# Kernel tuning notes

Hardware: AMD Instinct MI355X
Metric: run time of the kernel (lower is better)

Reference implementation:

```python
import jax, jax.numpy as jnp
import numpy as np

N, D, C, G, NNZ = 256, 1024, 50000, 4, 300000
EPS = 1e-5


def setup_inputs() -> dict:
    key = jax.random.key(0)
    ks = jax.random.split(key, 5)
    return {
        "output": jax.random.normal(ks[0], (N, D), jnp.float32),
        "wt2_w": jax.random.normal(ks[1], (C, D), jnp.float32) * 0.02,
        "wt2_b": jnp.zeros((C,), jnp.float32),
        "A_vals": jax.random.uniform(ks[2], (G, NNZ), dtype=jnp.float32),
        "vec": jnp.ones((G,), jnp.float32),
        "A_rows": jax.random.randint(ks[3], (G, NNZ), 0, C, jnp.int32),
        "A_cols": jax.random.randint(ks[4], (G, NNZ), 0, C, jnp.int32),
    }


def reference(output, wt2_w, wt2_b, A_vals, vec, A_rows, A_cols):
    # BatchNorm1d(embed_dim, affine=False), training-mode batch stats (biased var)
    mean = jnp.mean(output, axis=0)
    var = jnp.var(output, axis=0)
    h0 = (output - mean) * jax.lax.rsqrt(var + EPS)
    # wt2 linear + swish -> Z [N, C]
    h1 = h0 @ wt2_w.T + wt2_b
    Z = h1 * jax.nn.sigmoid(h1)
    # multi-graph sparse propagation: neighbors += spmm(A_i * vec[i], Z^T)^T
    # spmm out[b, r] = sum_{e: rows[e]==r} vals[e] * Z[b, cols[e]]
    Zt = Z.T  # [C, N]
    neighbors = jnp.zeros_like(Z)
    n_graphs = A_vals.shape[0]
    for i in range(n_graphs):  # small fixed number of relation graphs
        vals = A_vals[i] * vec[i]               # learnable per-graph weight
        msgs = Zt[A_cols[i]] * vals[:, None]    # [nnz, N] gathered messages
        agg = jax.ops.segment_sum(msgs, A_rows[i], num_segments=Zt.shape[0])  # [C, N]
        neighbors = neighbors + agg.T
    # residual combine
    return neighbors + Z
```

## Files before the change

kernel.cpp:

```cpp
#include <hip/hip_runtime.h>

typedef __attribute__((ext_vector_type(8))) short short8;
typedef __attribute__((ext_vector_type(4))) float floatx4;

#define C_DIM 50000
#define D_DIM 1024
#define N_DIM 256
#define G_NUM 4
#define NNZ_G 300000
#define E_TOT (G_NUM * NNZ_G)

#define O_SB   0u
#define O_H0   8192u
#define O_ZT   532480u
#define O_CNT  26132480u
#define O_OFF  26332544u
#define O_CUR  26532608u
#define O_BS   26732672u
#define O_EDG  26733696u

static __device__ __forceinline__ unsigned short f2bf(float f) {
    union { float f; unsigned u; } v; v.f = f;
    unsigned r = v.u + 0x7fffu + ((v.u >> 16) & 1u);
    return (unsigned short)(r >> 16);
}
static __device__ __forceinline__ float bf2f(unsigned short u) {
    union { unsigned u; float f; } v; v.u = ((unsigned)u) << 16;
    return v.f;
}

__global__ __launch_bounds__(256) void k_bnstats(const float* __restrict__ x,
                                                 float* __restrict__ scale,
                                                 float* __restrict__ bias) {
    int d = blockIdx.x * 256 + threadIdx.x;
    float s = 0.f, ss = 0.f;
    for (int n = 0; n < N_DIM; ++n) {
        float v = x[n * D_DIM + d];
        s += v; ss += v * v;
    }
    float mean = s * (1.f / N_DIM);
    float var  = ss * (1.f / N_DIM) - mean * mean;
    float sc = rsqrtf(var + 1e-5f);
    scale[d] = sc;
    bias[d] = -mean * sc;
}

__global__ __launch_bounds__(256) void k_h0(const float* __restrict__ x,
                                            const float* __restrict__ scale,
                                            const float* __restrict__ bias,
                                            unsigned short* __restrict__ h0) {
    int id = blockIdx.x * 256 + threadIdx.x;
    int d = id & (D_DIM - 1);
    h0[id] = f2bf(x[id] * scale[d] + bias[d]);
}

__global__ __launch_bounds__(256) void k_gemm(const float* __restrict__ W,
                                              const float* __restrict__ wb,
                                              const unsigned short* __restrict__ h0,
                                              unsigned short* __restrict__ Zt) {
    __shared__ unsigned short As[64 * 40];
    __shared__ unsigned short Bs[256 * 40];
    const int t = threadIdx.x;
    const int c0 = blockIdx.x * 64;
    const int w = t >> 6, lane = t & 63;
    const int m = lane & 15, g = lane >> 4;
    const int arow = t >> 2, aseg = t & 3;

    floatx4 acc[4][4];
#pragma unroll
    for (int i = 0; i < 4; ++i)
#pragma unroll
        for (int j = 0; j < 4; ++j) acc[i][j] = (floatx4)0.f;

    for (int kk = 0; kk < D_DIM; kk += 32) {
        {
            int c = c0 + arow;
            float4 f0, f1;
            if (c < C_DIM) {
                const float4* src = (const float4*)&W[(size_t)c * D_DIM + kk + aseg * 8];
                f0 = src[0]; f1 = src[1];
            } else {
                f0 = f1 = make_float4(0.f, 0.f, 0.f, 0.f);
            }
            unsigned p0 = (unsigned)f2bf(f0.x) | ((unsigned)f2bf(f0.y) << 16);
            unsigned p1 = (unsigned)f2bf(f0.z) | ((unsigned)f2bf(f0.w) << 16);
            unsigned p2 = (unsigned)f2bf(f1.x) | ((unsigned)f2bf(f1.y) << 16);
            unsigned p3 = (unsigned)f2bf(f1.z) | ((unsigned)f2bf(f1.w) << 16);
            *(uint4*)&As[arow * 40 + aseg * 8] = make_uint4(p0, p1, p2, p3);
        }
        {
            const uint4* src = (const uint4*)&h0[(size_t)t * D_DIM + kk];
            uint4* dst = (uint4*)&Bs[t * 40];
            dst[0] = src[0]; dst[1] = src[1]; dst[2] = src[2]; dst[3] = src[3];
        }
        __syncthreads();

        short8 af[4], bfr[4];
#pragma unroll
        for (int i = 0; i < 4; ++i)
            af[i] = *(const short8*)&As[(i * 16 + m) * 40 + g * 8];
#pragma unroll
        for (int j = 0; j < 4; ++j)
            bfr[j] = *(const short8*)&Bs[(w * 64 + j * 16 + m) * 40 + g * 8];
#pragma unroll
        for (int i = 0; i < 4; ++i)
#pragma unroll
            for (int j = 0; j < 4; ++j)
                acc[i][j] = __builtin_amdgcn_mfma_f32_16x16x32_bf16(af[i], bfr[j], acc[i][j], 0, 0, 0);
        __syncthreads();
    }

#pragma unroll
    for (int i = 0; i < 4; ++i) {
#pragma unroll
        for (int j = 0; j < 4; ++j) {
            int b = w * 64 + j * 16 + m;
#pragma unroll
            for (int rr = 0; rr < 4; ++rr) {
                int c = c0 + i * 16 + g * 4 + rr;
                if (c < C_DIM) {
                    float x = acc[i][j][rr] + wb[c];
                    float z = x / (1.f + __expf(-x));
                    Zt[(size_t)c * 256 + b] = f2bf(z);
                }
            }
        }
    }
}

__global__ __launch_bounds__(256) void k_count(const int* __restrict__ rows,
                                               int* __restrict__ counts) {
    int id = blockIdx.x * 256 + threadIdx.x;
    if (id < E_TOT) atomicAdd(&counts[rows[id]], 1);
}

__global__ __launch_bounds__(256) void k_scan1(const int* __restrict__ counts,
                                               int* __restrict__ offsets,
                                               int* __restrict__ bsums) {
    __shared__ int sm[256];
    int t = threadIdx.x, i = blockIdx.x * 256 + t;
    int v = (i < C_DIM) ? counts[i] : 0;
    sm[t] = v; __syncthreads();
    for (int off = 1; off < 256; off <<= 1) {
        int x = (t >= off) ? sm[t - off] : 0;
        __syncthreads();
        sm[t] += x;
        __syncthreads();
    }
    if (i < C_DIM) offsets[i] = sm[t] - v;
    if (t == 255) bsums[blockIdx.x] = sm[255];
}

__global__ __launch_bounds__(256) void k_scan2(int* __restrict__ bsums,
                                               int* __restrict__ offsets) {
    __shared__ int sm[256];
    int t = threadIdx.x;
    int v = (t < 196) ? bsums[t] : 0;
    sm[t] = v; __syncthreads();
    for (int off = 1; off < 256; off <<= 1) {
        int x = (t >= off) ? sm[t - off] : 0;
        __syncthreads();
        sm[t] += x;
        __syncthreads();
    }
    if (t < 196) bsums[t] = sm[t] - v;
    if (t == 0) offsets[C_DIM] = sm[255];
}

__global__ __launch_bounds__(256) void k_scan3(const int* __restrict__ bsums,
                                               int* __restrict__ offsets,
                                               int* __restrict__ cursor) {
    int i = blockIdx.x * 256 + threadIdx.x;
    if (i < C_DIM) {
        int off = offsets[i] + bsums[blockIdx.x];
        offsets[i] = off;
        cursor[i] = off;
    }
}

__global__ __launch_bounds__(256) void k_scatter(const int* __restrict__ rows,
                                                 const int* __restrict__ cols,
                                                 const float* __restrict__ vals,
                                                 const float* __restrict__ vec,
                                                 int* __restrict__ cursor,
                                                 int2* __restrict__ edges) {
    int id = blockIdx.x * 256 + threadIdx.x;
    if (id < E_TOT) {
        int gidx = id / NNZ_G;
        float v = vals[id] * vec[gidx];
        int r = rows[id];
        int c = cols[id];
        int pos = atomicAdd(&cursor[r], 1);
        edges[pos] = make_int2(c, __float_as_int(v));
    }
}

__global__ __launch_bounds__(256) void k_agg(const unsigned short* __restrict__ Zt,
                                             const int* __restrict__ offsets,
                                             const int2* __restrict__ edges,
                                             float* __restrict__ out) {
    __shared__ float sm[32 * 256];
    const int t = threadIdx.x;
    const int w = t >> 6, lane = t & 63;
    const int r0 = blockIdx.x * 32;
    const int base = lane * 4;

#pragma unroll 1
    for (int k = 0; k < 8; ++k) {
        int lrow = w * 8 + k;
        int r = __builtin_amdgcn_readfirstlane(r0 + lrow);
        if (r < C_DIM) {
            ushort4 z = *(const ushort4*)&Zt[(size_t)r * 256 + base];
            float a0 = bf2f(z.x), a1 = bf2f(z.y), a2 = bf2f(z.z), a3 = bf2f(z.w);
            int s = offsets[r], e = offsets[r + 1];
            for (; s + 4 <= e; s += 4) {
                int2 e0 = edges[s], e1 = edges[s + 1], e2 = edges[s + 2], e3 = edges[s + 3];
                ushort4 g0 = *(const ushort4*)&Zt[(size_t)e0.x * 256 + base];
                ushort4 g1 = *(const ushort4*)&Zt[(size_t)e1.x * 256 + base];
                ushort4 g2 = *(const ushort4*)&Zt[(size_t)e2.x * 256 + base];
                ushort4 g3 = *(const ushort4*)&Zt[(size_t)e3.x * 256 + base];
                float v0 = __int_as_float(e0.y), v1 = __int_as_float(e1.y);
                float v2 = __int_as_float(e2.y), v3 = __int_as_float(e3.y);
                a0 += v0 * bf2f(g0.x) + v1 * bf2f(g1.x) + v2 * bf2f(g2.x) + v3 * bf2f(g3.x);
                a1 += v0 * bf2f(g0.y) + v1 * bf2f(g1.y) + v2 * bf2f(g2.y) + v3 * bf2f(g3.y);
                a2 += v0 * bf2f(g0.z) + v1 * bf2f(g1.z) + v2 * bf2f(g2.z) + v3 * bf2f(g3.z);
                a3 += v0 * bf2f(g0.w) + v1 * bf2f(g1.w) + v2 * bf2f(g2.w) + v3 * bf2f(g3.w);
            }
            for (; s < e; ++s) {
                int2 e0 = edges[s];
                ushort4 g0 = *(const ushort4*)&Zt[(size_t)e0.x * 256 + base];
                float v0 = __int_as_float(e0.y);
                a0 += v0 * bf2f(g0.x);
                a1 += v0 * bf2f(g0.y);
                a2 += v0 * bf2f(g0.z);
                a3 += v0 * bf2f(g0.w);
            }
            *(float4*)&sm[lrow * 256 + base] = make_float4(a0, a1, a2, a3);
        }
    }
    __syncthreads();

    int rows = C_DIM - r0; if (rows > 32) rows = 32;
    int nq = rows >> 2;
    float4* op = (float4*)&out[(size_t)t * C_DIM + r0];
#pragma unroll 1
    for (int q = 0; q < nq; ++q) {
        float4 o;
        o.x = sm[(q * 4 + 0) * 256 + t];
        o.y = sm[(q * 4 + 1) * 256 + t];
        o.z = sm[(q * 4 + 2) * 256 + t];
        o.w = sm[(q * 4 + 3) * 256 + t];
        op[q] = o;
    }
}

extern "C" void kernel_launch(void* const* d_in, const int* in_sizes, int n_in,
                              void* d_out, int out_size, void* d_ws, size_t ws_size,
                              hipStream_t stream) {
    (void)in_sizes; (void)n_in; (void)out_size; (void)ws_size;
    const float* x     = (const float*)d_in[0];
    const float* W     = (const float*)d_in[1];
    const float* wb    = (const float*)d_in[2];
    const float* Avals = (const float*)d_in[3];
    const float* vec   = (const float*)d_in[4];
    const int*   Arows = (const int*)d_in[5];
    const int*   Acols = (const int*)d_in[6];
    float* out = (float*)d_out;
    char* ws = (char*)d_ws;

    float* scale = (float*)(ws + O_SB);
    float* bias  = scale + 1024;
    unsigned short* h0 = (unsigned short*)(ws + O_H0);
    unsigned short* Zt = (unsigned short*)(ws + O_ZT);
    int* counts  = (int*)(ws + O_CNT);
    int* offsets = (int*)(ws + O_OFF);
    int* cursor  = (int*)(ws + O_CUR);
    int* bsums   = (int*)(ws + O_BS);
    int2* edges  = (int2*)(ws + O_EDG);

    hipMemsetAsync(counts, 0, C_DIM * sizeof(int), stream);

    k_bnstats<<<4, 256, 0, stream>>>(x, scale, bias);
    k_h0<<<1024, 256, 0, stream>>>(x, scale, bias, h0);
    k_count<<<(E_TOT + 255) / 256, 256, 0, stream>>>(Arows, counts);
    k_gemm<<<(C_DIM + 63) / 64, 256, 0, stream>>>(W, wb, h0, Zt);
    k_scan1<<<196, 256, 0, stream>>>(counts, offsets, bsums);
    k_scan2<<<1, 256, 0, stream>>>(bsums, offsets);
    k_scan3<<<196, 256, 0, stream>>>(bsums, offsets, cursor);
    k_scatter<<<(E_TOT + 255) / 256, 256, 0, stream>>>(Arows, Acols, Avals, vec, cursor, edges);
    k_agg<<<(C_DIM + 31) / 32, 256, 0, stream>>>(Zt, offsets, edges, out);
}
```

Measured before the change: 663.4 us.

## Double-buffer W tile in LDS and read h0 fragments directly from global

Restructures the GEMM main loop to use a K-step of 64 with a double-buffered LDS tile for W, stored in fragment-native order so each lane reads its MFMA operand contiguously. The h0 operand is no longer staged through LDS; each wave loads its B fragments straight from global memory. The next W tile is prefetched into registers during the MFMAs, which halves the barriers per K and aims to overlap global latency with compute. In exchange, h0 is reread from global/L2 by every block, and out-of-range rows are clamped rather than zeroed, which is safe only because those outputs are masked on store.

```diff
diff --git a/kernel.cpp b/kernel.cpp
--- a/kernel.cpp
+++ b/kernel.cpp
@@ -29,6 +29,15 @@
     return v.f;
 }
 
+static __device__ __forceinline__ short8 cvt8(float4 a, float4 b) {
+    short8 r;
+    r[0] = (short)f2bf(a.x); r[1] = (short)f2bf(a.y);
+    r[2] = (short)f2bf(a.z); r[3] = (short)f2bf(a.w);
+    r[4] = (short)f2bf(b.x); r[5] = (short)f2bf(b.y);
+    r[6] = (short)f2bf(b.z); r[7] = (short)f2bf(b.w);
+    return r;
+}
+
 __global__ __launch_bounds__(256) void k_bnstats(const float* __restrict__ x,
                                                  float* __restrict__ scale,
                                                  float* __restrict__ bias) {
@@ -58,13 +67,20 @@
                                               const float* __restrict__ wb,
                                               const unsigned short* __restrict__ h0,
                                               unsigned short* __restrict__ Zt) {
-    __shared__ unsigned short As[64 * 40];
-    __shared__ unsigned short Bs[256 * 40];
+    __shared__ unsigned short A_lds[2][8 * 64 * 8];
     const int t = threadIdx.x;
-    const int c0 = blockIdx.x * 64;
     const int w = t >> 6, lane = t & 63;
     const int m = lane & 15, g = lane >> 4;
-    const int arow = t >> 2, aseg = t & 3;
+    const int c0 = blockIdx.x * 64;
+
+    const int p0 = 2 * w, p1 = 2 * w + 1;
+    int r0s = c0 + (p0 & 3) * 16 + m; if (r0s >= C_DIM) r0s = C_DIM - 1;
+    int r1s = c0 + (p1 & 3) * 16 + m; if (r1s >= C_DIM) r1s = C_DIM - 1;
+    const float* srcA0 = &W[(size_t)r0s * D_DIM + (p0 >> 2) * 32 + g * 8];
+    const float* srcA1 = &W[(size_t)r1s * D_DIM + (p1 >> 2) * 32 + g * 8];
+    unsigned short* dst0base = &A_lds[0][0];
+
+    const unsigned short* hb = h0 + (size_t)(w * 64 + m) * D_DIM;
 
     floatx4 acc[4][4];
 #pragma unroll
@@ -72,43 +88,61 @@
 #pragma unroll
         for (int j = 0; j < 4; ++j) acc[i][j] = (floatx4)0.f;
 
-    for (int kk = 0; kk < D_DIM; kk += 32) {
-        {
-            int c = c0 + arow;
-            float4 f0, f1;
-            if (c < C_DIM) {
-                const float4* src = (const float4*)&W[(size_t)c * D_DIM + kk + aseg * 8];
-                f0 = src[0]; f1 = src[1];
-            } else {
-                f0 = f1 = make_float4(0.f, 0.f, 0.f, 0.f);
-            }
-            unsigned p0 = (unsigned)f2bf(f0.x) | ((unsigned)f2bf(f0.y) << 16);
-            unsigned p1 = (unsigned)f2bf(f0.z) | ((unsigned)f2bf(f0.w) << 16);
-            unsigned p2 = (unsigned)f2bf(f1.x) | ((unsigned)f2bf(f1.y) << 16);
-            unsigned p3 = (unsigned)f2bf(f1.z) | ((unsigned)f2bf(f1.w) << 16);
-            *(uint4*)&As[arow * 40 + aseg * 8] = make_uint4(p0, p1, p2, p3);
-        }
-        {
-            const uint4* src = (const uint4*)&h0[(size_t)t * D_DIM + kk];
-            uint4* dst = (uint4*)&Bs[t * 40];
-            dst[0] = src[0]; dst[1] = src[1]; dst[2] = src[2]; dst[3] = src[3];
-        }
-        __syncthreads();
-
-        short8 af[4], bfr[4];
-#pragma unroll
-        for (int i = 0; i < 4; ++i)
-            af[i] = *(const short8*)&As[(i * 16 + m) * 40 + g * 8];
-#pragma unroll
-        for (int j = 0; j < 4; ++j)
-            bfr[j] = *(const short8*)&Bs[(w * 64 + j * 16 + m) * 40 + g * 8];
-#pragma unroll
-        for (int i = 0; i < 4; ++i)
+    float4 pa0, pa1, pb0, pb1;
+
+#define LOADA(kkv)                                              \
+    {                                                           \
+        const float4* sa = (const float4*)(srcA0 + (kkv));      \
+        const float4* sb = (const float4*)(srcA1 + (kkv));      \
+        pa0 = sa[0]; pa1 = sa[1];                               \
+        pb0 = sb[0]; pb1 = sb[1];                               \
+    }
+#define STOREA(bufv)                                                        \
+    {                                                                       \
+        *(short8*)&A_lds[(bufv)][p0 * 512 + lane * 8] = cvt8(pa0, pa1);     \
+        *(short8*)&A_lds[(bufv)][p1 * 512 + lane * 8] = cvt8(pb0, pb1);     \
+    }
+
+    LOADA(0);
+    STOREA(0);
+    __syncthreads();
+
+    int cur = 0;
+#pragma unroll 1
+    for (int ks = 0; ks < 16; ++ks) {
+        const int kk = ks * 64;
+        short8 bfrag[2][4];
+#pragma unroll
+        for (int kh = 0; kh < 2; ++kh)
 #pragma unroll
             for (int j = 0; j < 4; ++j)
-                acc[i][j] = __builtin_amdgcn_mfma_f32_16x16x32_bf16(af[i], bfr[j], acc[i][j], 0, 0, 0);
-        __syncthreads();
-    }
+                bfrag[kh][j] = *(const short8*)&hb[(size_t)(j * 16) * D_DIM + kk + kh * 32 + g * 8];
+
+        if (ks < 15) LOADA(kk + 64);
+
+        short8 afrag[2][4];
+#pragma unroll
+        for (int kh = 0; kh < 2; ++kh)
+#pragma unroll
+            for (int i = 0; i < 4; ++i)
+                afrag[kh][i] = *(const short8*)&A_lds[cur][(kh * 4 + i) * 512 + lane * 8];
+
+        __builtin_amdgcn_s_setprio(1);
+#pragma unroll
+        for (int kh = 0; kh < 2; ++kh)
+#pragma unroll
+            for (int i = 0; i < 4; ++i)
+#pragma unroll
+                for (int j = 0; j < 4; ++j)
+                    acc[i][j] = __builtin_amdgcn_mfma_f32_16x16x32_bf16(afrag[kh][i], bfrag[kh][j], acc[i][j], 0, 0, 0);
+        __builtin_amdgcn_s_setprio(0);
+
+        if (ks < 15) STOREA(cur ^ 1);
+        __syncthreads();
+        cur ^= 1;
+    }
+#undef LOADA
+#undef STOREA
 
 #pragma unroll
     for (int i = 0; i < 4; ++i) {
@@ -126,6 +160,7 @@
             }
         }
     }
+    (void)dst0base;
 }
 
 __global__ __launch_bounds__(256) void k_count(const int* __restrict__ rows,
```

New measurement: 636.9 us. 1.04x faster.
